# Kernel tuning notes

Hardware: AMD Instinct MI355X
Metric: run time of the kernel (lower is better)

The kernel has to match this reference:

```python
import jax, jax.numpy as jnp
import numpy as np

B, N, D = 64, 256, 768
ITER_STEPS = 1


def _linear_w(key, out_d, in_d):
    s = 1.0 / np.sqrt(in_d)
    return jax.random.uniform(key, (out_d, in_d), jnp.float32, -s, s)


def setup_inputs() -> dict:
    key = jax.random.key(0)
    ks = jax.random.split(key, 16)
    node = jax.random.normal(ks[0], (B, N, D), jnp.float32)
    node_mask = jnp.ones((B, N), jnp.int32)
    argument_graph = jax.random.randint(ks[1], (B, N, N), 0, 2, jnp.int32)
    punctuation_graph = jax.random.randint(ks[2], (B, N, N), 0, 2, jnp.int32)
    inp = {
        "node": node,
        "node_mask": node_mask,
        "argument_graph": argument_graph,
        "punctuation_graph": punctuation_graph,
        # node-relatedness scorer: Linear(D, 1, bias=True)
        "Wq": _linear_w(ks[3], 1, D),
        "bq": jnp.zeros((1,), jnp.float32),
        # self node fc: Linear(D, D, bias=True)
        "Ws": _linear_w(ks[4], D, D),
        "bs": jnp.zeros((D,), jnp.float32),
        # 8 relation projections, Linear(D, D, bias=False)
        "Wa": _linear_w(ks[5], D, D),
        "Wp": _linear_w(ks[6], D, D),
        "Wap": _linear_w(ks[7], D, D),
        "Wpp": _linear_w(ks[8], D, D),
        "Wa2": _linear_w(ks[9], D, D),
        "Wp2": _linear_w(ks[10], D, D),
        "Wap2": _linear_w(ks[11], D, D),
        "Wpp2": _linear_w(ks[12], D, D),
    }
    return inp


def reference(node, node_mask, argument_graph, punctuation_graph,
              Wq, bq, Ws, bs, Wa, Wp, Wap, Wpp, Wa2, Wp2, Wap2, Wpp2):
    f32 = jnp.float32
    mask = node_mask.astype(f32)                      # [B, N]
    n = node.shape[1]
    eye = jnp.eye(n, dtype=f32)
    # dd_graph: node_mask outer product with zeroed diagonal
    dd = mask[:, None, :] * mask[:, :, None] * (1.0 - eye)   # [B, N, N]
    g_a = dd * argument_graph.astype(f32)
    g_p = dd * punctuation_graph.astype(f32)
    # reverse directed edges
    g_ar = dd * jnp.swapaxes(g_a, 1, 2)
    g_pr = dd * jnp.swapaxes(g_p, 1, 2)
    neigh = g_a.sum(-1) + g_p.sum(-1) + g_ar.sum(-1) + g_pr.sum(-1)  # [B, N]
    denom = jnp.where(neigh >= 1.0, neigh, 1.0)

    all_weight = []
    for _ in range(ITER_STEPS):
        # (1) node relatedness
        dw = jax.nn.sigmoid(jnp.einsum('bnd,od->bno', node, Wq) + bq)[..., 0]  # [B, N]
        all_weight.append(dw)
        self_info = jnp.einsum('bnd,ed->bne', node, Ws) + bs

        def msg(g, W):
            # node_weight: broadcast dw over rows, zero where no edge
            nw = dw[:, None, :] * g                    # [B, N, N]
            proj = jnp.einsum('bnd,ed->bne', node, W)  # [B, N, D]
            return jnp.matmul(nw, proj)                # [B, N, D]

        agg = (msg(g_a, Wa) + msg(g_p, Wp) + msg(g_ar, Wap) + msg(g_pr, Wpp)
               + msg(g_a, Wa2) + msg(g_p, Wp2) + msg(g_ar, Wap2) + msg(g_pr, Wpp2))
        agg = agg / denom[..., None]
        # (3) node update
        node = jax.nn.relu(self_info + agg)

    all_weight = jnp.stack(all_weight, axis=1)  # [B, steps, N]
    return node, all_weight
```

## Files before the change

kernel.cpp:

```cpp
#include <hip/hip_runtime.h>
#include <hip/hip_bf16.h>
#include <math.h>

typedef __bf16 bf16;
typedef unsigned char u8;
typedef __bf16 bf16x8 __attribute__((ext_vector_type(8)));
typedef float f32x4 __attribute__((ext_vector_type(4)));

#define BB 64
#define NN 256
#define DD 768
#define MM (BB*NN)
#define KP 1024
#define WSZ (DD*DD)
#define TL 144

__device__ __forceinline__ void async16(const void* g, void* l) {
  __builtin_amdgcn_global_load_lds((__attribute__((address_space(1))) void*)g,
                                   (__attribute__((address_space(3))) void*)l,
                                   16, 0, 0);
}

__device__ __forceinline__ void stage_tile(const bf16* gsrc, int ld, char* ldst,
                                           int wv, int lane) {
#pragma unroll
  for (int cc = 0; cc < 2; ++cc) {
    int c = wv * 2 + cc;
    int row = c * 16 + (lane >> 2);
    int col = (lane & 3) * 8;
    async16(gsrc + (size_t)row * ld + col, ldst + c * 1024);
  }
}

__device__ __forceinline__ void stage_fp8(const u8* gsrc, int ld, char* ldst,
                                          int wv, int lane) {
  int row = wv * 32 + (lane >> 1);
  int col = (lane & 1) * 16;
  async16(gsrc + (size_t)row * ld + col, ldst + wv * 1024);
}

__device__ __forceinline__ void mma_step(const char* lA, const char* lB,
                                         f32x4 acc[4][4], int lane, int wr, int wc) {
  bf16x8 af[4], bfr[4];
  int rbase = wr * 64 + (lane & 15);
  int cbase = wc * 64 + (lane & 15);
  int ko = (lane >> 4) * 8;
#pragma unroll
  for (int r = 0; r < 4; ++r)
    af[r] = *(const bf16x8*)(lA + (((rbase + r * 16) * 32) + ko) * 2);
#pragma unroll
  for (int c = 0; c < 4; ++c)
    bfr[c] = *(const bf16x8*)(lB + (((cbase + c * 16) * 32) + ko) * 2);
#pragma unroll
  for (int r = 0; r < 4; ++r)
#pragma unroll
    for (int c = 0; c < 4; ++c)
      acc[r][c] = __builtin_amdgcn_mfma_f32_16x16x32_bf16(af[r], bfr[c], acc[r][c], 0, 0, 0);
}

__device__ __forceinline__ void mma_step_fp8(const char* lA, const char* lB,
                                             f32x4 acc[4][4], int lane, int wr, int wc) {
  long af[4], bfr[4];
  int rbase = wr * 64 + (lane & 15);
  int cbase = wc * 64 + (lane & 15);
  int ko = (lane >> 4) * 8;
#pragma unroll
  for (int r = 0; r < 4; ++r)
    af[r] = *(const long*)(lA + (rbase + r * 16) * 32 + ko);
#pragma unroll
  for (int c = 0; c < 4; ++c)
    bfr[c] = *(const long*)(lB + (cbase + c * 16) * 32 + ko);
#pragma unroll
  for (int r = 0; r < 4; ++r)
#pragma unroll
    for (int c = 0; c < 4; ++c)
      acc[r][c] = __builtin_amdgcn_mfma_f32_16x16x32_fp8_fp8(af[r], bfr[c], acc[r][c], 0, 0, 0);
}

__device__ __forceinline__ void k_step64(const bf16* Ab, int lda, const bf16* Bb, int ldb,
                                         char* smem, f32x4 acc[4][4],
                                         int wv, int lane, int wr, int wc) {
  char* lA0 = smem;
  char* lA1 = smem + 8192;
  char* lB0 = smem + 16384;
  char* lB1 = smem + 24576;
  __syncthreads();
  stage_tile(Ab, lda, lA0, wv, lane);
  stage_tile(Ab + 32, lda, lA1, wv, lane);
  stage_tile(Bb, ldb, lB0, wv, lane);
  stage_tile(Bb + 32, ldb, lB1, wv, lane);
  __builtin_amdgcn_s_waitcnt(0);
  __syncthreads();
  mma_step(lA0, lB0, acc, lane, wr, wc);
  mma_step(lA1, lB1, acc, lane, wr, wc);
}

__device__ __forceinline__ unsigned pack4(float a, float b, float c, float d) {
  int w = 0;
  w = __builtin_amdgcn_cvt_pk_fp8_f32(a, b, w, false);
  w = __builtin_amdgcn_cvt_pk_fp8_f32(c, d, w, true);
  return (unsigned)w;
}

__global__ void k_pre(const float* __restrict__ node, const float* __restrict__ Wq,
                      const float* __restrict__ bq, bf16* __restrict__ node_bf,
                      float* __restrict__ dw, float* __restrict__ allw,
                      float* __restrict__ neigh,
                      const float* __restrict__ Ws,
                      const float* __restrict__ Wa, const float* __restrict__ Wp,
                      const float* __restrict__ Wap, const float* __restrict__ Wpp,
                      const float* __restrict__ Wa2, const float* __restrict__ Wp2,
                      const float* __restrict__ Wap2, const float* __restrict__ Wpp2,
                      bf16* __restrict__ Wcat4, bf16* __restrict__ Ws_bf) {
  if (blockIdx.x < MM / 4) {
    int lane = threadIdx.x & 63, wv = threadIdx.x >> 6;
    int row = blockIdx.x * 4 + wv;
    const float* nr = node + (size_t)row * DD;
    bf16* nb = node_bf + (size_t)row * DD;
    float s = 0.f;
#pragma unroll
    for (int k = 0; k < DD / 64; ++k) {
      int idx = lane + k * 64;
      float v = nr[idx];
      nb[idx] = (bf16)v;
      s += v * Wq[idx];
    }
#pragma unroll
    for (int off = 32; off; off >>= 1) s += __shfl_down(s, off);
    if (lane == 0) {
      float z = s + bq[0];
      float d = 1.f / (1.f + expf(-z));
      dw[row] = d;
      allw[row] = d;
      neigh[row] = 0.f;
    }
  } else {
    int i = (blockIdx.x - MM / 4) * 256 + threadIdx.x;
    Ws_bf[i] = (bf16)Ws[i];
    Wcat4[i]           = (bf16)(Wa[i] + Wa2[i]);
    Wcat4[i + WSZ]     = (bf16)(Wp[i] + Wp2[i]);
    Wcat4[i + 2 * WSZ] = (bf16)(Wap[i] + Wap2[i]);
    Wcat4[i + 3 * WSZ] = (bf16)(Wpp[i] + Wpp2[i]);
  }
}

__global__ void k_graph(const int* __restrict__ mask, const int* __restrict__ arg,
                        const int* __restrict__ pun, const float* __restrict__ dw,
                        u8* __restrict__ g8, float* __restrict__ neigh) {
  __shared__ float la[64][65];
  __shared__ float lp[64][65];
  __shared__ float msk[256];
  __shared__ float dwv[256];
  int tid = threadIdx.x;
  int bi = blockIdx.x;
  int b = bi >> 4, it = (bi >> 2) & 3, jt = bi & 3;
  int i0 = it * 64, j0 = jt * 64;
  msk[tid] = (float)mask[b * NN + tid];
  dwv[tid] = dw[b * NN + tid];
  __syncthreads();
  int ir = tid >> 2, c4 = (tid & 3) * 16;
  int i = i0 + ir;
  float mi = msk[i];
  size_t gb = (size_t)b * NN * NN;
  const int* ap = arg + gb + (size_t)i * NN + j0 + c4;
  const int* pp = pun + gb + (size_t)i * NN + j0 + c4;
  float va[16], vp[16];
  float racc = 0.f;
#pragma unroll
  for (int k = 0; k < 16; ++k) {
    int j = j0 + c4 + k;
    float dd = (i == j) ? 0.f : mi * msk[j];
    float ga = dd * (float)ap[k];
    float gp = dd * (float)pp[k];
    la[ir][c4 + k] = ga;
    lp[ir][c4 + k] = gp;
    float w = dwv[j];
    va[k] = w * ga;
    vp[k] = w * gp;
    racc += ga + gp;
  }
  uint4 oa, op;
#pragma unroll
  for (int g = 0; g < 4; ++g) {
    (&oa.x)[g] = pack4(va[g*4], va[g*4+1], va[g*4+2], va[g*4+3]);
    (&op.x)[g] = pack4(vp[g*4], vp[g*4+1], vp[g*4+2], vp[g*4+3]);
  }
  *(uint4*)(g8 + (size_t)(b * NN + i) * KP + 0 * NN + j0 + c4) = oa;
  *(uint4*)(g8 + (size_t)(b * NN + i) * KP + 1 * NN + j0 + c4) = op;
  racc += __shfl_xor(racc, 1);
  racc += __shfl_xor(racc, 2);
  if ((tid & 3) == 0) atomicAdd(&neigh[b * NN + i], racc);
  __syncthreads();
  int jr = ir, ic4 = c4;
  float cacc = 0.f;
#pragma unroll
  for (int k = 0; k < 16; ++k) {
    float ga = la[ic4 + k][jr];
    float gp = lp[ic4 + k][jr];
    float w = dwv[i0 + ic4 + k];
    va[k] = w * ga;
    vp[k] = w * gp;
    cacc += ga + gp;
  }
#pragma unroll
  for (int g = 0; g < 4; ++g) {
    (&oa.x)[g] = pack4(va[g*4], va[g*4+1], va[g*4+2], va[g*4+3]);
    (&op.x)[g] = pack4(vp[g*4], vp[g*4+1], vp[g*4+2], vp[g*4+3]);
  }
  *(uint4*)(g8 + (size_t)(b * NN + j0 + jr) * KP + 2 * NN + i0 + ic4) = oa;
  *(uint4*)(g8 + (size_t)(b * NN + j0 + jr) * KP + 3 * NN + i0 + ic4) = op;
  cacc += __shfl_xor(cacc, 1);
  cacc += __shfl_xor(cacc, 2);
  if ((tid & 3) == 0) atomicAdd(&neigh[b * NN + j0 + jr], cacc);
}

__global__ __launch_bounds__(256) void k_proj(const bf16* __restrict__ node_bf,
                                              const bf16* __restrict__ Wcat4,
                                              u8* __restrict__ p8) {
  __shared__ __align__(16) char smem[32768];
  int tid = threadIdx.x, lane = tid & 63, wv = tid >> 6, wr = wv >> 1, wc = wv & 1;
  int m0 = blockIdx.x * 128;
  int n0 = blockIdx.y * 128;
  const bf16* Ab = node_bf + (size_t)m0 * DD;
  const bf16* Bb = Wcat4 + (size_t)n0 * DD;
  f32x4 z = {0.f, 0.f, 0.f, 0.f};
  f32x4 acc[4][4];
#pragma unroll
  for (int r = 0; r < 4; ++r)
#pragma unroll
    for (int c = 0; c < 4; ++c) acc[r][c] = z;
  for (int k0 = 0; k0 < DD; k0 += 64)
    k_step64(Ab + k0, DD, Bb + k0, DD, smem, acc, wv, lane, wr, wc);
  __syncthreads();
  int b = m0 >> 8, j0 = m0 & 255;
  int X = n0 / DD, e0 = n0 - X * DD;
  u8* tb = (u8*)smem;
#pragma unroll
  for (int r = 0; r < 4; ++r)
#pragma unroll
    for (int c = 0; c < 4; ++c) {
      int n = wc * 64 + c * 16 + (lane & 15);
      int m = wr * 64 + r * 16 + ((lane >> 4) << 2);
      *(unsigned*)(tb + n * TL + m) =
          pack4(acc[r][c][0], acc[r][c][1], acc[r][c][2], acc[r][c][3]);
    }
  __syncthreads();
  u8* obase = p8 + ((size_t)b * DD + e0) * KP + X * NN + j0;
#pragma unroll
  for (int t = 0; t < 4; ++t) {
    int row = t * 32 + (tid >> 3);
    int col = (tid & 7) * 16;
    uint4 v = *(const uint4*)(tb + row * TL + col);
    *(uint4*)(obase + (size_t)row * KP + col) = v;
  }
}

__global__ __launch_bounds__(256) void k_agg(const u8* __restrict__ g8,
                                             const u8* __restrict__ p8,
                                             const bf16* __restrict__ node_bf,
                                             const bf16* __restrict__ Ws_bf,
                                             const float* __restrict__ neigh,
                                             const float* __restrict__ bs,
                                             float* __restrict__ out) {
  __shared__ __align__(16) char smem[32768];
  int tid = threadIdx.x, lane = tid & 63, wv = tid >> 6, wr = wv >> 1, wc = wv & 1;
  int l = blockIdx.x;
  int xcd = l & 7, idx = l >> 3;
  int b = (idx / 12) * 8 + xcd;
  int t = idx % 12;
  int i0 = (t / 6) * 128, e0 = (t % 6) * 128;
  f32x4 z = {0.f, 0.f, 0.f, 0.f};
  f32x4 acc[4][4];
#pragma unroll
  for (int r = 0; r < 4; ++r)
#pragma unroll
    for (int c = 0; c < 4; ++c) acc[r][c] = z;
  const u8* Ab = g8 + (size_t)(b * NN + i0) * KP;
  const u8* Bb = p8 + ((size_t)b * DD + e0) * KP;
  for (int k0 = 0; k0 < KP; k0 += 128) {
    __syncthreads();
#pragma unroll
    for (int s = 0; s < 4; ++s) {
      stage_fp8(Ab + k0 + s * 32, KP, smem + s * 4096, wv, lane);
      stage_fp8(Bb + k0 + s * 32, KP, smem + 16384 + s * 4096, wv, lane);
    }
    __builtin_amdgcn_s_waitcnt(0);
    __syncthreads();
#pragma unroll
    for (int s = 0; s < 4; ++s)
      mma_step_fp8(smem + s * 4096, smem + 16384 + s * 4096, acc, lane, wr, wc);
  }
  int rowb = i0 + wr * 64 + (lane >> 4) * 4;
#pragma unroll
  for (int r = 0; r < 4; ++r)
#pragma unroll
    for (int q = 0; q < 4; ++q) {
      float rd = 1.f / fmaxf(neigh[b * NN + rowb + r * 16 + q], 1.f);
#pragma unroll
      for (int c = 0; c < 4; ++c) acc[r][c][q] *= rd;
    }
  const bf16* Ab2 = node_bf + (size_t)(b * NN + i0) * DD;
  const bf16* Bb2 = Ws_bf + (size_t)e0 * DD;
  for (int k0 = 0; k0 < DD; k0 += 64)
    k_step64(Ab2 + k0, DD, Bb2 + k0, DD, smem, acc, wv, lane, wr, wc);
  int colb = e0 + wc * 64 + (lane & 15);
#pragma unroll
  for (int c = 0; c < 4; ++c) {
    int col = colb + c * 16;
    float bv = bs[col];
#pragma unroll
    for (int r = 0; r < 4; ++r)
#pragma unroll
      for (int q = 0; q < 4; ++q) {
        int m = b * NN + rowb + r * 16 + q;
        out[(size_t)m * DD + col] = fmaxf(acc[r][c][q] + bv, 0.f);
      }
  }
}

extern "C" void kernel_launch(void* const* d_in, const int* in_sizes, int n_in,
                              void* d_out, int out_size, void* d_ws, size_t ws_size,
                              hipStream_t stream) {
  const float* node = (const float*)d_in[0];
  const int* mask   = (const int*)d_in[1];
  const int* arg    = (const int*)d_in[2];
  const int* pun    = (const int*)d_in[3];
  const float* Wq   = (const float*)d_in[4];
  const float* bq   = (const float*)d_in[5];
  const float* Ws   = (const float*)d_in[6];
  const float* bs   = (const float*)d_in[7];
  const float* Wa   = (const float*)d_in[8];
  const float* Wp   = (const float*)d_in[9];
  const float* Wap  = (const float*)d_in[10];
  const float* Wpp  = (const float*)d_in[11];
  const float* Wa2  = (const float*)d_in[12];
  const float* Wp2  = (const float*)d_in[13];
  const float* Wap2 = (const float*)d_in[14];
  const float* Wpp2 = (const float*)d_in[15];

  float* out  = (float*)d_out;
  float* allw = out + (size_t)MM * DD;

  char* ws = (char*)d_ws;
  bf16* node_bf = (bf16*)ws;
  float* dw     = (float*)(ws + 25165824);
  float* neigh  = (float*)(ws + 25231360);
  bf16* Wcat4   = (bf16*)(ws + 25296896);
  bf16* Ws_bf   = (bf16*)(ws + 30015488);
  u8*   g8      = (u8*)(ws + 31195136);
  u8*   p8      = (u8*)(ws + 47972352);
  (void)ws_size; (void)in_sizes; (void)n_in; (void)out_size;

  k_pre<<<MM / 4 + WSZ / 256, 256, 0, stream>>>(node, Wq, bq, node_bf, dw, allw, neigh,
                                                Ws, Wa, Wp, Wap, Wpp,
                                                Wa2, Wp2, Wap2, Wpp2, Wcat4, Ws_bf);
  k_graph<<<BB * 16, 256, 0, stream>>>(mask, arg, pun, dw, g8, neigh);
  k_proj<<<dim3(128, 24), 256, 0, stream>>>(node_bf, Wcat4, p8);
  k_agg<<<12 * BB, 256, 0, stream>>>(g8, p8, node_bf, Ws_bf, neigh, bs, out);
}
```

Measured before the change: 330.6 us.

## Fuse graph build and projection GEMM into one interleaved kernel

Merges k_graph and k_proj into a single k_mid launch where every fourth block builds graph tiles and the other blocks compute projection tiles, so the memory-bound graph work overlaps the compute-bound GEMM. The dw node weight moves from the graph side to the projection epilogue: graph entries are now stored as plain 0/1 in fp8 (exact), and dw scales the projected rows before fp8 packing. The transpose buffer in LDS shrinks to bf16. This removes one kernel boundary and makes the graph values exact, but it adds a branch with unequal per-block work and changes where the fp8 rounding happens.

New measurement: 363.6 us. +10.0%, slower.

```diff
diff --git a/kernel.cpp b/kernel.cpp
--- a/kernel.cpp
+++ b/kernel.cpp
@@ -144,83 +144,86 @@
   }
 }
 
-__global__ void k_graph(const int* __restrict__ mask, const int* __restrict__ arg,
-                        const int* __restrict__ pun, const float* __restrict__ dw,
-                        u8* __restrict__ g8, float* __restrict__ neigh) {
-  __shared__ float la[64][65];
-  __shared__ float lp[64][65];
-  __shared__ float msk[256];
-  __shared__ float dwv[256];
+__global__ __launch_bounds__(256) void k_mid(const int* __restrict__ mask,
+                                             const int* __restrict__ arg,
+                                             const int* __restrict__ pun,
+                                             const float* __restrict__ dw,
+                                             const bf16* __restrict__ node_bf,
+                                             const bf16* __restrict__ Wcat4,
+                                             u8* __restrict__ g8,
+                                             float* __restrict__ neigh,
+                                             u8* __restrict__ p8) {
+  __shared__ __align__(16) char smem[32768];
   int tid = threadIdx.x;
-  int bi = blockIdx.x;
-  int b = bi >> 4, it = (bi >> 2) & 3, jt = bi & 3;
-  int i0 = it * 64, j0 = jt * 64;
-  msk[tid] = (float)mask[b * NN + tid];
-  dwv[tid] = dw[b * NN + tid];
-  __syncthreads();
-  int ir = tid >> 2, c4 = (tid & 3) * 16;
-  int i = i0 + ir;
-  float mi = msk[i];
-  size_t gb = (size_t)b * NN * NN;
-  const int* ap = arg + gb + (size_t)i * NN + j0 + c4;
-  const int* pp = pun + gb + (size_t)i * NN + j0 + c4;
-  float va[16], vp[16];
-  float racc = 0.f;
-#pragma unroll
-  for (int k = 0; k < 16; ++k) {
-    int j = j0 + c4 + k;
-    float dd = (i == j) ? 0.f : mi * msk[j];
-    float ga = dd * (float)ap[k];
-    float gp = dd * (float)pp[k];
-    la[ir][c4 + k] = ga;
-    lp[ir][c4 + k] = gp;
-    float w = dwv[j];
-    va[k] = w * ga;
-    vp[k] = w * gp;
-    racc += ga + gp;
-  }
-  uint4 oa, op;
-#pragma unroll
-  for (int g = 0; g < 4; ++g) {
-    (&oa.x)[g] = pack4(va[g*4], va[g*4+1], va[g*4+2], va[g*4+3]);
-    (&op.x)[g] = pack4(vp[g*4], vp[g*4+1], vp[g*4+2], vp[g*4+3]);
-  }
-  *(uint4*)(g8 + (size_t)(b * NN + i) * KP + 0 * NN + j0 + c4) = oa;
-  *(uint4*)(g8 + (size_t)(b * NN + i) * KP + 1 * NN + j0 + c4) = op;
-  racc += __shfl_xor(racc, 1);
-  racc += __shfl_xor(racc, 2);
-  if ((tid & 3) == 0) atomicAdd(&neigh[b * NN + i], racc);
-  __syncthreads();
-  int jr = ir, ic4 = c4;
-  float cacc = 0.f;
-#pragma unroll
-  for (int k = 0; k < 16; ++k) {
-    float ga = la[ic4 + k][jr];
-    float gp = lp[ic4 + k][jr];
-    float w = dwv[i0 + ic4 + k];
-    va[k] = w * ga;
-    vp[k] = w * gp;
-    cacc += ga + gp;
-  }
-#pragma unroll
-  for (int g = 0; g < 4; ++g) {
-    (&oa.x)[g] = pack4(va[g*4], va[g*4+1], va[g*4+2], va[g*4+3]);
-    (&op.x)[g] = pack4(vp[g*4], vp[g*4+1], vp[g*4+2], vp[g*4+3]);
-  }
-  *(uint4*)(g8 + (size_t)(b * NN + j0 + jr) * KP + 2 * NN + i0 + ic4) = oa;
-  *(uint4*)(g8 + (size_t)(b * NN + j0 + jr) * KP + 3 * NN + i0 + ic4) = op;
-  cacc += __shfl_xor(cacc, 1);
-  cacc += __shfl_xor(cacc, 2);
-  if ((tid & 3) == 0) atomicAdd(&neigh[b * NN + j0 + jr], cacc);
-}
-
-__global__ __launch_bounds__(256) void k_proj(const bf16* __restrict__ node_bf,
-                                              const bf16* __restrict__ Wcat4,
-                                              u8* __restrict__ p8) {
-  __shared__ __align__(16) char smem[32768];
-  int tid = threadIdx.x, lane = tid & 63, wv = tid >> 6, wr = wv >> 1, wc = wv & 1;
-  int m0 = blockIdx.x * 128;
-  int n0 = blockIdx.y * 128;
+  int s = blockIdx.x & 3, g = blockIdx.x >> 2;
+
+  if (s == 3) {
+    bf16* la = (bf16*)smem;
+    bf16* lp = la + 64 * 66;
+    float* msk = (float*)(lp + 64 * 66);
+    int b = g >> 4, it = (g >> 2) & 3, jt = g & 3;
+    int i0 = it * 64, j0 = jt * 64;
+    msk[tid] = (float)mask[b * NN + tid];
+    __syncthreads();
+    int ir = tid >> 2, c4 = (tid & 3) * 16;
+    int i = i0 + ir;
+    float mi = msk[i];
+    size_t gb = (size_t)b * NN * NN;
+    const int* ap = arg + gb + (size_t)i * NN + j0 + c4;
+    const int* pp = pun + gb + (size_t)i * NN + j0 + c4;
+    float va[16], vp[16];
+    float racc = 0.f;
+#pragma unroll
+    for (int k = 0; k < 16; ++k) {
+      int j = j0 + c4 + k;
+      float dd = (i == j) ? 0.f : mi * msk[j];
+      float ga = dd * (float)ap[k];
+      float gp = dd * (float)pp[k];
+      la[ir * 66 + c4 + k] = (bf16)ga;
+      lp[ir * 66 + c4 + k] = (bf16)gp;
+      va[k] = ga;
+      vp[k] = gp;
+      racc += ga + gp;
+    }
+    uint4 oa, op;
+#pragma unroll
+    for (int q = 0; q < 4; ++q) {
+      (&oa.x)[q] = pack4(va[q*4], va[q*4+1], va[q*4+2], va[q*4+3]);
+      (&op.x)[q] = pack4(vp[q*4], vp[q*4+1], vp[q*4+2], vp[q*4+3]);
+    }
+    *(uint4*)(g8 + (size_t)(b * NN + i) * KP + 0 * NN + j0 + c4) = oa;
+    *(uint4*)(g8 + (size_t)(b * NN + i) * KP + 1 * NN + j0 + c4) = op;
+    racc += __shfl_xor(racc, 1);
+    racc += __shfl_xor(racc, 2);
+    if ((tid & 3) == 0) atomicAdd(&neigh[b * NN + i], racc);
+    __syncthreads();
+    int jr = ir, ic4 = c4;
+    float cacc = 0.f;
+#pragma unroll
+    for (int k = 0; k < 16; ++k) {
+      float ga = (float)la[(ic4 + k) * 66 + jr];
+      float gp = (float)lp[(ic4 + k) * 66 + jr];
+      va[k] = ga;
+      vp[k] = gp;
+      cacc += ga + gp;
+    }
+#pragma unroll
+    for (int q = 0; q < 4; ++q) {
+      (&oa.x)[q] = pack4(va[q*4], va[q*4+1], va[q*4+2], va[q*4+3]);
+      (&op.x)[q] = pack4(vp[q*4], vp[q*4+1], vp[q*4+2], vp[q*4+3]);
+    }
+    *(uint4*)(g8 + (size_t)(b * NN + j0 + jr) * KP + 2 * NN + i0 + ic4) = oa;
+    *(uint4*)(g8 + (size_t)(b * NN + j0 + jr) * KP + 3 * NN + i0 + ic4) = op;
+    cacc += __shfl_xor(cacc, 1);
+    cacc += __shfl_xor(cacc, 2);
+    if ((tid & 3) == 0) atomicAdd(&neigh[b * NN + j0 + jr], cacc);
+    return;
+  }
+
+  int p = g * 3 + s;
+  int m0 = (p % 128) * 128;
+  int n0 = (p / 128) * 128;
+  int lane = tid & 63, wv = tid >> 6, wr = wv >> 1, wc = wv & 1;
   const bf16* Ab = node_bf + (size_t)m0 * DD;
   const bf16* Bb = Wcat4 + (size_t)n0 * DD;
   f32x4 z = {0.f, 0.f, 0.f, 0.f};
@@ -236,14 +239,17 @@
   int X = n0 / DD, e0 = n0 - X * DD;
   u8* tb = (u8*)smem;
 #pragma unroll
-  for (int r = 0; r < 4; ++r)
+  for (int r = 0; r < 4; ++r) {
+    int mb = wr * 64 + r * 16 + ((lane >> 4) << 2);
+    f32x4 dv = *(const f32x4*)(dw + b * NN + j0 + mb);
 #pragma unroll
     for (int c = 0; c < 4; ++c) {
       int n = wc * 64 + c * 16 + (lane & 15);
-      int m = wr * 64 + r * 16 + ((lane >> 4) << 2);
-      *(unsigned*)(tb + n * TL + m) =
-          pack4(acc[r][c][0], acc[r][c][1], acc[r][c][2], acc[r][c][3]);
-    }
+      *(unsigned*)(tb + n * TL + mb) =
+          pack4(acc[r][c][0] * dv[0], acc[r][c][1] * dv[1],
+                acc[r][c][2] * dv[2], acc[r][c][3] * dv[3]);
+    }
+  }
   __syncthreads();
   u8* obase = p8 + ((size_t)b * DD + e0) * KP + X * NN + j0;
 #pragma unroll
@@ -280,15 +286,15 @@
   for (int k0 = 0; k0 < KP; k0 += 128) {
     __syncthreads();
 #pragma unroll
-    for (int s = 0; s < 4; ++s) {
-      stage_fp8(Ab + k0 + s * 32, KP, smem + s * 4096, wv, lane);
-      stage_fp8(Bb + k0 + s * 32, KP, smem + 16384 + s * 4096, wv, lane);
+    for (int ss = 0; ss < 4; ++ss) {
+      stage_fp8(Ab + k0 + ss * 32, KP, smem + ss * 4096, wv, lane);
+      stage_fp8(Bb + k0 + ss * 32, KP, smem + 16384 + ss * 4096, wv, lane);
     }
     __builtin_amdgcn_s_waitcnt(0);
     __syncthreads();
 #pragma unroll
-    for (int s = 0; s < 4; ++s)
-      mma_step_fp8(smem + s * 4096, smem + 16384 + s * 4096, acc, lane, wr, wc);
+    for (int ss = 0; ss < 4; ++ss)
+      mma_step_fp8(smem + ss * 4096, smem + 16384 + ss * 4096, acc, lane, wr, wc);
   }
   int rowb = i0 + wr * 64 + (lane >> 4) * 4;
 #pragma unroll
@@ -351,10 +357,9 @@
   u8*   p8      = (u8*)(ws + 47972352);
   (void)ws_size; (void)in_sizes; (void)n_in; (void)out_size;
 
-  k_pre<<<MM / 4 + WSZ / 256, 256, 0, stream>>>(node, Wq, bq, node_bf, dw, allw, neigh,
-                                                Ws, Wa, Wp, Wap, Wpp,
+  k_pre<<<MM / 4 + WSZ / 256, 256, 0, stream>>>(node, Wq, bq, node_bf, dw, allw,
+                                                neigh, Ws, Wa, Wp, Wap, Wpp,
                                                 Wa2, Wp2, Wap2, Wpp2, Wcat4, Ws_bf);
-  k_graph<<<BB * 16, 256, 0, stream>>>(mask, arg, pun, dw, g8, neigh);
-  k_proj<<<dim3(128, 24), 256, 0, stream>>>(node_bf, Wcat4, p8);
+  k_mid<<<4096, 256, 0, stream>>>(mask, arg, pun, dw, node_bf, Wcat4, g8, neigh, p8);
   k_agg<<<12 * BB, 256, 0, stream>>>(g8, p8, node_bf, Ws_bf, neigh, bs, out);
 }
```

## Store fp8 graph and projection operands in pre-tiled MFMA-friendly layout

Applied to the files above, without the earlier changes.

The fp8 adjacency (g8) and projected features (p8) are now written by k_graph and k_proj into 4KB tiles arranged as k-octet-major blocks of 128 rows. k_agg can then stage each tile with one contiguous 16-byte load per lane and read MFMA fragments with simple strided LDS addresses. The aim is to improve global load coalescing and reduce LDS bank conflicts in the aggregation GEMM. In exchange, the producer kernels' stores become scattered 8-byte writes, which may cost more write efficiency.

Result: no change. 329.5 us (-0.4%).

```diff
diff --git a/kernel.cpp b/kernel.cpp
--- a/kernel.cpp
+++ b/kernel.cpp
@@ -4,6 +4,7 @@
 
 typedef __bf16 bf16;
 typedef unsigned char u8;
+typedef unsigned long long ull;
 typedef __bf16 bf16x8 __attribute__((ext_vector_type(8)));
 typedef float f32x4 __attribute__((ext_vector_type(4)));
 
@@ -15,6 +16,7 @@
 #define WSZ (DD*DD)
 #define TL 144
 
+
 __device__ __forceinline__ void async16(const void* g, void* l) {
   __builtin_amdgcn_global_load_lds((__attribute__((address_space(1))) void*)g,
                                    (__attribute__((address_space(3))) void*)l,
@@ -30,13 +32,6 @@
     int col = (lane & 3) * 8;
     async16(gsrc + (size_t)row * ld + col, ldst + c * 1024);
   }
-}
-
-__device__ __forceinline__ void stage_fp8(const u8* gsrc, int ld, char* ldst,
-                                          int wv, int lane) {
-  int row = wv * 32 + (lane >> 1);
-  int col = (lane & 1) * 16;
-  async16(gsrc + (size_t)row * ld + col, ldst + wv * 1024);
 }
 
 __device__ __forceinline__ void mma_step(const char* lA, const char* lB,
@@ -58,18 +53,18 @@
       acc[r][c] = __builtin_amdgcn_mfma_f32_16x16x32_bf16(af[r], bfr[c], acc[r][c], 0, 0, 0);
 }
 
-__device__ __forceinline__ void mma_step_fp8(const char* lA, const char* lB,
-                                             f32x4 acc[4][4], int lane, int wr, int wc) {
+__device__ __forceinline__ void mma_step_fp8t(const char* lA, const char* lB,
+                                              f32x4 acc[4][4], int lane, int wr, int wc) {
   long af[4], bfr[4];
-  int rbase = wr * 64 + (lane & 15);
-  int cbase = wc * 64 + (lane & 15);
-  int ko = (lane >> 4) * 8;
-#pragma unroll
-  for (int r = 0; r < 4; ++r)
-    af[r] = *(const long*)(lA + (rbase + r * 16) * 32 + ko);
+  int koq = (lane >> 4) * 1024;
+  int mA = (wr * 64 + (lane & 15)) * 8;
+  int mB = (wc * 64 + (lane & 15)) * 8;
+#pragma unroll
+  for (int r = 0; r < 4; ++r)
+    af[r] = *(const long*)(lA + koq + mA + r * 128);
 #pragma unroll
   for (int c = 0; c < 4; ++c)
-    bfr[c] = *(const long*)(lB + (cbase + c * 16) * 32 + ko);
+    bfr[c] = *(const long*)(lB + koq + mB + c * 128);
 #pragma unroll
   for (int r = 0; r < 4; ++r)
 #pragma unroll
@@ -144,6 +139,12 @@
   }
 }
 
+__device__ __forceinline__ void store_tiled(u8* base, int tile, int kin, int m, uint4 v) {
+  size_t o = (size_t)tile * 4096 + (size_t)((kin >> 3) * 1024 + m * 8);
+  *(ull*)(base + o)        = ((ull)v.y << 32) | v.x;
+  *(ull*)(base + o + 1024) = ((ull)v.w << 32) | v.z;
+}
+
 __global__ void k_graph(const int* __restrict__ mask, const int* __restrict__ arg,
                         const int* __restrict__ pun, const float* __restrict__ dw,
                         u8* __restrict__ g8, float* __restrict__ neigh) {
@@ -185,8 +186,12 @@
     (&oa.x)[g] = pack4(va[g*4], va[g*4+1], va[g*4+2], va[g*4+3]);
     (&op.x)[g] = pack4(vp[g*4], vp[g*4+1], vp[g*4+2], vp[g*4+3]);
   }
-  *(uint4*)(g8 + (size_t)(b * NN + i) * KP + 0 * NN + j0 + c4) = oa;
-  *(uint4*)(g8 + (size_t)(b * NN + i) * KP + 1 * NN + j0 + c4) = op;
+  {
+    int tR = (b * 2 + (i >> 7)) * 32;
+    int K0 = j0 + c4;
+    store_tiled(g8, tR + (K0 >> 5),       K0 & 31, i & 127, oa);
+    store_tiled(g8, tR + 8 + (K0 >> 5),   K0 & 31, i & 127, op);
+  }
   racc += __shfl_xor(racc, 1);
   racc += __shfl_xor(racc, 2);
   if ((tid & 3) == 0) atomicAdd(&neigh[b * NN + i], racc);
@@ -207,8 +212,13 @@
     (&oa.x)[g] = pack4(va[g*4], va[g*4+1], va[g*4+2], va[g*4+3]);
     (&op.x)[g] = pack4(vp[g*4], vp[g*4+1], vp[g*4+2], vp[g*4+3]);
   }
-  *(uint4*)(g8 + (size_t)(b * NN + j0 + jr) * KP + 2 * NN + i0 + ic4) = oa;
-  *(uint4*)(g8 + (size_t)(b * NN + j0 + jr) * KP + 3 * NN + i0 + ic4) = op;
+  {
+    int row = j0 + jr;
+    int tR = (b * 2 + (row >> 7)) * 32;
+    int K2 = i0 + ic4;
+    store_tiled(g8, tR + 16 + (K2 >> 5),  K2 & 31, row & 127, oa);
+    store_tiled(g8, tR + 24 + (K2 >> 5),  K2 & 31, row & 127, op);
+  }
   cacc += __shfl_xor(cacc, 1);
   cacc += __shfl_xor(cacc, 2);
   if ((tid & 3) == 0) atomicAdd(&neigh[b * NN + j0 + jr], cacc);
@@ -245,13 +255,14 @@
           pack4(acc[r][c][0], acc[r][c][1], acc[r][c][2], acc[r][c][3]);
     }
   __syncthreads();
-  u8* obase = p8 + ((size_t)b * DD + e0) * KP + X * NN + j0;
+  int tR = (b * 6 + (e0 >> 7)) * 32 + X * 8;
 #pragma unroll
   for (int t = 0; t < 4; ++t) {
     int row = t * 32 + (tid >> 3);
     int col = (tid & 7) * 16;
     uint4 v = *(const uint4*)(tb + row * TL + col);
-    *(uint4*)(obase + (size_t)row * KP + col) = v;
+    int K = j0 + col;
+    store_tiled(p8, tR + (K >> 5), K & 31, row, v);
   }
 }
 
@@ -275,20 +286,23 @@
   for (int r = 0; r < 4; ++r)
 #pragma unroll
     for (int c = 0; c < 4; ++c) acc[r][c] = z;
-  const u8* Ab = g8 + (size_t)(b * NN + i0) * KP;
-  const u8* Bb = p8 + ((size_t)b * DD + e0) * KP;
+  const u8* At = g8 + (size_t)((b * 2 + (i0 >> 7)) * 32) * 4096;
+  const u8* Bt = p8 + (size_t)((b * 6 + (e0 >> 7)) * 32) * 4096;
+  int lsoff = wv * 1024;
+  int goff = lsoff + lane * 16;
   for (int k0 = 0; k0 < KP; k0 += 128) {
     __syncthreads();
 #pragma unroll
     for (int s = 0; s < 4; ++s) {
-      stage_fp8(Ab + k0 + s * 32, KP, smem + s * 4096, wv, lane);
-      stage_fp8(Bb + k0 + s * 32, KP, smem + 16384 + s * 4096, wv, lane);
+      size_t toff = (size_t)((k0 >> 5) + s) * 4096 + goff;
+      async16(At + toff, smem + s * 4096 + lsoff);
+      async16(Bt + toff, smem + 16384 + s * 4096 + lsoff);
     }
     __builtin_amdgcn_s_waitcnt(0);
     __syncthreads();
 #pragma unroll
     for (int s = 0; s < 4; ++s)
-      mma_step_fp8(smem + s * 4096, smem + 16384 + s * 4096, acc, lane, wr, wc);
+      mma_step_fp8t(smem + s * 4096, smem + 16384 + s * 4096, acc, lane, wr, wc);
   }
   int rowb = i0 + wr * 64 + (lane >> 4) * 4;
 #pragma unroll
@@ -351,8 +365,8 @@
   u8*   p8      = (u8*)(ws + 47972352);
   (void)ws_size; (void)in_sizes; (void)n_in; (void)out_size;
 
-  k_pre<<<MM / 4 + WSZ / 256, 256, 0, stream>>>(node, Wq, bq, node_bf, dw, allw, neigh,
-                                                Ws, Wa, Wp, Wap, Wpp,
+  k_pre<<<MM / 4 + WSZ / 256, 256, 0, stream>>>(node, Wq, bq, node_bf, dw, allw,
+                                                neigh, Ws, Wa, Wp, Wap, Wpp,
                                                 Wa2, Wp2, Wap2, Wpp2, Wcat4, Ws_bf);
   k_graph<<<BB * 16, 256, 0, stream>>>(mask, arg, pun, dw, g8, neigh);
   k_proj<<<dim3(128, 24), 256, 0, stream>>>(node_bf, Wcat4, p8);
```
